# Performance work log

Hardware: AMD Instinct MI355X
Metric: run time of the kernel (lower is better)

Reference implementation:

```python
import jax, jax.numpy as jnp
from jax import lax
import numpy as np

N_TAGS = 16      # number of pos-tag experts
N_PRI = 4        # first N_PRI tags are privacy terms
UNK_ID = 0
VOCAB = 40000    # parser word vocabulary
M = 1024         # per-tag target vocab size
E = 100          # parser embedding dim
WED = 200        # word embedding dim (input encoder)
PED = 56         # pos embedding dim (input encoder)
H = 512          # ctx_fs (per-direction LSTM hidden)
TEMP = 1.0       # eval-mode gumbel temperature
ENT_PEN = 0.01


def _lstm(x, mask, Wx, Wh, b, reverse):
    # x: [B, L, D], mask: [B, L]; returns hidden states [B, L, H]
    B = x.shape[0]
    Hd = Wh.shape[0]
    gates_x = jnp.einsum('bld,dg->blg', x, Wx) + b  # precompute input part of gates

    def step(carry, inp):
        h, c = carry
        gx, m = inp  # gx: [B, 4H], m: [B, 1]
        gates = gx + h @ Wh
        i, f, g, o = jnp.split(gates, 4, axis=-1)
        i = jax.nn.sigmoid(i)
        f = jax.nn.sigmoid(f)
        g = jnp.tanh(g)
        o = jax.nn.sigmoid(o)
        c_new = f * c + i * g
        h_new = o * jnp.tanh(c_new)
        # masked update (padded steps keep previous state)
        h_new = h_new * m + h * (1.0 - m)
        c_new = c_new * m + c * (1.0 - m)
        return (h_new, c_new), h_new

    seq = (jnp.swapaxes(gates_x, 0, 1), jnp.swapaxes(mask, 0, 1)[..., None])
    init = (jnp.zeros((B, Hd), x.dtype), jnp.zeros((B, Hd), x.dtype))
    _, hs = lax.scan(step, init, seq, reverse=reverse)
    return jnp.swapaxes(hs, 0, 1)


def setup_inputs():
    key = jax.random.key(0)
    ks = jax.random.split(key, 16)
    B, L = 32, 256
    D = WED + PED  # 256
    inp = {}
    inp['inp_word'] = jax.random.randint(ks[0], (B, L), 0, VOCAB, dtype=jnp.int32)
    inp['inp_pos'] = jax.random.randint(ks[1], (B, L), 0, N_TAGS, dtype=jnp.int32)
    inp['inp_mask'] = jnp.ones((B, L), jnp.float32)
    inp['gumbel_u'] = jax.random.uniform(ks[2], (B * L, M), jnp.float32)
    inp['word_emb'] = jax.random.normal(ks[3], (VOCAB, WED), jnp.float32) * 0.1
    inp['pos_emb'] = jax.random.normal(ks[4], (N_TAGS, PED), jnp.float32) * 0.1
    inp['Wx_f'] = jax.random.normal(ks[5], (D, 4 * H), jnp.float32) * 0.05
    inp['Wh_f'] = jax.random.normal(ks[6], (H, 4 * H), jnp.float32) * 0.05
    inp['b_f'] = jnp.zeros((4 * H,), jnp.float32)
    inp['Wx_b'] = jax.random.normal(ks[7], (D, 4 * H), jnp.float32) * 0.05
    inp['Wh_b'] = jax.random.normal(ks[8], (H, 4 * H), jnp.float32) * 0.05
    inp['b_b'] = jnp.zeros((4 * H,), jnp.float32)
    inp['dec_W'] = jax.random.normal(ks[9], (N_TAGS, 2 * H, M), jnp.float32) * 0.03
    inp['dec_b'] = jnp.zeros((N_TAGS, M), jnp.float32)
    inp['words_tbl'] = jax.random.randint(ks[10], (N_TAGS, M), 0, VOCAB, dtype=jnp.int32)
    inp['psr_weight'] = jax.random.normal(ks[11], (VOCAB, E), jnp.float32) * 0.1
    return inp


def reference(inp_word, inp_pos, inp_mask, gumbel_u, word_emb, pos_emb,
              Wx_f, Wh_f, b_f, Wx_b, Wh_b, b_b, dec_W, dec_b, words_tbl, psr_weight):
    B, L = inp_word.shape
    # input encoder: word + pos embedding concat
    x = jnp.concatenate([word_emb[inp_word], pos_emb[inp_pos]], axis=-1)
    # bidirectional masked LSTM context
    hf = _lstm(x, inp_mask, Wx_f, Wh_f, b_f, reverse=False)
    hb = _lstm(x, inp_mask, Wx_b, Wh_b, b_b, reverse=True)
    ctx = jnp.concatenate([hf, hb], axis=-1).reshape(B * L, 2 * H)

    pos = inp_pos.reshape(-1)            # [T]
    wflat = inp_word.reshape(-1)         # [T]
    g = -jnp.log(-jnp.log(gumbel_u + 1e-10) + 1e-10)  # gumbel noise [T, M]

    obf_word = wflat
    obf_emb = psr_weight[wflat]          # [T, E]
    entropy = jnp.float32(0.0)
    for p in range(N_TAGS):  # loop over fixed small expert set
        m = pos == p                                    # routing mask [T]
        logp = jax.nn.log_softmax(ctx @ dec_W[p] + dec_b[p], axis=-1)  # [T, M]
        n = jnp.sum(m).astype(logp.dtype)
        ent_p = jnp.sum((-logp * jnp.exp(logp)) * m[:, None]) / jnp.maximum(n * M, 1.0)
        entropy = entropy + jnp.where(n > 0, ent_p, 0.0)
        spt = jax.nn.softmax((logp + g) / TEMP, axis=-1)  # gumbel-softmax sample
        widx = words_tbl[p][jnp.argmax(spt, axis=-1)]
        obf_word = jnp.where(m, widx, obf_word)
        emb = spt @ psr_weight[words_tbl[p]]              # [T, E]
        obf_emb = jnp.where(m[:, None], emb, obf_emb)

    obf_mask = pos < N_TAGS   # all tags are target tags
    pri_mask = pos < N_PRI
    avoid = (obf_word == wflat) & obf_mask
    obf_word = jnp.where(avoid, UNK_ID, obf_word)
    obf_emb = jnp.where(avoid[:, None], psr_weight[UNK_ID], obf_emb)
    ent_loss = -entropy * ENT_PEN
    return (obf_word.reshape(B, L), obf_emb.reshape(B, L, E),
            obf_mask.reshape(B, L), pri_mask.reshape(B, L), ent_loss)
```

## Files before the change

kernel.cpp:

```cpp
#include <hip/hip_runtime.h>
#include <math.h>
#include <cstdint>

#define BB 32
#define LL 256
#define TT 8192
#define DIN 256
#define WEDm 200
#define PEDm 56
#define HH 512
#define G4 2048
#define MM 1024
#define EE 100
#define NTAGS 16

__global__ void k_embed(const int* __restrict__ word, const int* __restrict__ posi,
                        const float* __restrict__ wemb, const float* __restrict__ pemb,
                        float* __restrict__ X) {
  int t = blockIdx.x;
  int c = threadIdx.x * 4;
  float4 v;
  if (c < WEDm) {
    int w = word[t];
    v = *(const float4*)(wemb + (size_t)w * WEDm + c);
  } else {
    int p = posi[t];
    v = *(const float4*)(pemb + (size_t)p * PEDm + (c - WEDm));
  }
  *(float4*)(X + (size_t)t * DIN + c) = v;
}

__global__ __launch_bounds__(256) void k_gemm_bias(const float* __restrict__ A,
    const float* __restrict__ W, const float* __restrict__ bias,
    float* __restrict__ C, int Mm, int Nn, int Kk) {
  __shared__ float As[16][68];
  __shared__ float Bs[16][64];
  int tid = threadIdx.x;
  int tx = tid & 15, ty = tid >> 4;
  int row0 = blockIdx.y * 64, col0 = blockIdx.x * 64;
  float acc[4][4] = {};
  for (int k0 = 0; k0 < Kk; k0 += 16) {
    int r = tid >> 2, c = (tid & 3) * 4;
    float4 av = *(const float4*)(A + (size_t)(row0 + r) * Kk + k0 + c);
    As[c + 0][r] = av.x; As[c + 1][r] = av.y; As[c + 2][r] = av.z; As[c + 3][r] = av.w;
    int r2 = tid >> 4, c2 = (tid & 15) * 4;
    float4 bv = *(const float4*)(W + (size_t)(k0 + r2) * Nn + col0 + c2);
    *(float4*)(&Bs[r2][c2]) = bv;
    __syncthreads();
#pragma unroll
    for (int kk = 0; kk < 16; ++kk) {
      float4 a4 = *(const float4*)(&As[kk][ty * 4]);
      float4 b4 = *(const float4*)(&Bs[kk][tx * 4]);
      float a[4] = {a4.x, a4.y, a4.z, a4.w};
      float b[4] = {b4.x, b4.y, b4.z, b4.w};
#pragma unroll
      for (int i = 0; i < 4; ++i)
#pragma unroll
        for (int j = 0; j < 4; ++j)
          acc[i][j] += a[i] * b[j];
    }
    __syncthreads();
  }
#pragma unroll
  for (int i = 0; i < 4; ++i) {
    int row = row0 + ty * 4 + i;
#pragma unroll
    for (int j = 0; j < 4; ++j) {
      int col = col0 + tx * 4 + j;
      C[(size_t)row * Nn + col] = acc[i][j] + bias[col];
    }
  }
}

template <int N>
__device__ __forceinline__ float ror_add(float x) {
  int xi = __float_as_int(x);
  int yi = __builtin_amdgcn_update_dpp(xi, xi, 0x100 + N, 0xF, 0xF, false);
  return x + __int_as_float(yi);
}

__device__ __forceinline__ float sigm(float x) { return 1.f / (1.f + __expf(-x)); }

__global__ __launch_bounds__(512, 1) void k_lstm6(
    const float* __restrict__ Whf, const float* __restrict__ Whb,
    const float* __restrict__ GXfp, const float* __restrict__ GXbp,
    const float* __restrict__ maskp, float* __restrict__ Hbuf,
    float* __restrict__ ctx, int* __restrict__ flags) {
  extern __shared__ float lds[];
  float* Wtmp = lds;
  float* Hs   = lds;
  float* part = lds + 8 * 516;
  const int tid = threadIdx.x;
  const int wg  = blockIdx.x;
  const int dir = wg & 1;
  const int bg  = (wg >> 1) & 3;
  const int ug  = wg >> 3;
  const int j0  = ug * 16;
  const int b0  = bg * 8;
  const float* Wh = dir ? Whb : Whf;
  const float* GX = dir ? GXbp : GXfp;

  const int ks = tid & 31;
  const int cq = tid >> 5;
  const int uu = tid & 15, bloc = tid >> 4;

  float4 wreg[4][4];
#pragma unroll
  for (int cc = 0; cc < 4; ++cc) {
    for (int i = tid; i < 16 * 512; i += 512) {
      int c = i >> 9, k = i & 511;
      Wtmp[c * 512 + k] = Wh[(size_t)k * G4 + cc * HH + j0 + c];
    }
    __syncthreads();
    if ((cq >> 2) == cc) {
      int cbase = (cq & 3) * 4;
#pragma unroll
      for (int ci = 0; ci < 4; ++ci)
#pragma unroll
        for (int j = 0; j < 4; ++j)
          wreg[ci][j] = *(const float4*)(Wtmp + (cbase + ci) * 512 + 4 * ks + 128 * j);
    }
    __syncthreads();
  }

  if (tid < 128) {
    __hip_atomic_store(&Hbuf[(size_t)(0 * 2 + dir) * 16384 + (b0 + bloc) * HH + j0 + uu],
                       0.f, __ATOMIC_RELAXED, __HIP_MEMORY_SCOPE_AGENT);
  }
  asm volatile("s_waitcnt vmcnt(0)" ::: "memory");
  __syncthreads();
  if (tid == 0)
    __hip_atomic_store(&flags[wg], 1, __ATOMIC_RELAXED, __HIP_MEMORY_SCOPE_AGENT);

  float cstate = 0.f;
  int par = 0;

  for (int s = 0; s < LL; ++s) {
    const int t = dir ? (LL - 1 - s) : s;

    float gx0 = 0.f, gx1 = 0.f, gx2 = 0.f, gx3 = 0.f, mval = 0.f;
    if (tid < 128) {
      const float* gp = GX + ((size_t)((b0 + bloc) * LL + t)) * G4 + j0 + uu;
      gx0 = gp[0]; gx1 = gp[512]; gx2 = gp[1024]; gx3 = gp[1536];
      mval = maskp[(b0 + bloc) * LL + t];
    }

    if (tid < 32) {
      int it = 0;
      while (__hip_atomic_load(&flags[(tid * 4 + bg) * 2 + dir], __ATOMIC_RELAXED,
                               __HIP_MEMORY_SCOPE_AGENT) < s + 1) {
        __builtin_amdgcn_s_sleep(1);
        if (++it > (1 << 20)) break;
      }
    }
    __syncthreads();
    __builtin_amdgcn_sched_barrier(0);

    {
      const unsigned long long* hb64 =
          (const unsigned long long*)(Hbuf + (size_t)(par * 2 + dir) * 16384 + b0 * HH);
      unsigned long long hv[4];
#pragma unroll
      for (int m = 0; m < 4; ++m)
        hv[m] = __hip_atomic_load(&hb64[tid + 512 * m], __ATOMIC_RELAXED,
                                  __HIP_MEMORY_SCOPE_AGENT);
#pragma unroll
      for (int m = 0; m < 4; ++m) {
        int f = 2 * (tid + 512 * m);
        int b = f >> 9, k = f & 511;
        *(float2*)(&Hs[b * 516 + k]) = *(float2*)(&hv[m]);
      }
    }
    __syncthreads();

    float acc[4][8];
#pragma unroll
    for (int ci = 0; ci < 4; ++ci)
#pragma unroll
      for (int bi = 0; bi < 8; ++bi) acc[ci][bi] = 0.f;
    {
      const float* hp = Hs + 4 * ks;
#pragma unroll
      for (int j = 0; j < 4; ++j) {
        const int ko = 128 * j;
        float4 h4[8];
#pragma unroll
        for (int bi = 0; bi < 8; ++bi) h4[bi] = *(const float4*)(hp + bi * 516 + ko);
#pragma unroll
        for (int ci = 0; ci < 4; ++ci) {
          float4 w = wreg[ci][j];
#pragma unroll
          for (int bi = 0; bi < 8; ++bi) {
            float4 h = h4[bi];
            acc[ci][bi] += w.x * h.x + w.y * h.y + w.z * h.z + w.w * h.w;
          }
        }
      }
    }
#pragma unroll
    for (int ci = 0; ci < 4; ++ci)
#pragma unroll
      for (int bi = 0; bi < 8; ++bi) {
        float v = acc[ci][bi];
        v = ror_add<1>(v); v = ror_add<2>(v); v = ror_add<4>(v); v = ror_add<8>(v);
        acc[ci][bi] = v;
      }
    if ((ks & 15) == 0) {
      const int ph = ks >> 4;
      float* dst = part + ph * 768 + (cq * 4) * 12;
#pragma unroll
      for (int ci = 0; ci < 4; ++ci) {
        *(float4*)(dst + ci * 12 + 0) = make_float4(acc[ci][0], acc[ci][1], acc[ci][2], acc[ci][3]);
        *(float4*)(dst + ci * 12 + 4) = make_float4(acc[ci][4], acc[ci][5], acc[ci][6], acc[ci][7]);
      }
    }
    __syncthreads();

    float hn = 0.f;
    if (tid < 128) {
      float pre[4];
#pragma unroll
      for (int q = 0; q < 4; ++q) {
        int lc = q * 16 + uu;
        pre[q] = part[lc * 12 + bloc] + part[768 + lc * 12 + bloc];
      }
      pre[0] += gx0; pre[1] += gx1; pre[2] += gx2; pre[3] += gx3;
      float gi = sigm(pre[0]);
      float gf = sigm(pre[1]);
      float gg = tanhf(pre[2]);
      float go = sigm(pre[3]);
      float cnew = gf * cstate + gi * gg;
      float hnew = go * tanhf(cnew);
      float hold = Hs[bloc * 516 + j0 + uu];
      hn = hnew * mval + hold * (1.f - mval);
      cstate = cnew * mval + cstate * (1.f - mval);
      __hip_atomic_store(&Hbuf[(size_t)((par ^ 1) * 2 + dir) * 16384 + (b0 + bloc) * HH + j0 + uu],
                         hn, __ATOMIC_RELAXED, __HIP_MEMORY_SCOPE_AGENT);
    }
    asm volatile("s_waitcnt vmcnt(0)" ::: "memory");
    __syncthreads();
    if (tid == 0)
      __hip_atomic_store(&flags[wg], s + 2, __ATOMIC_RELAXED, __HIP_MEMORY_SCOPE_AGENT);
    if (tid < 128)
      ctx[((size_t)((b0 + bloc) * LL + t)) * (2 * HH) + dir * HH + j0 + uu] = hn;
    par ^= 1;
  }
}

__global__ void k_init0(int* __restrict__ flags) { flags[threadIdx.x] = 0; }

__global__ void k_zero16(int* counts) { if (threadIdx.x < 16) counts[threadIdx.x] = 0; }

__global__ void k_count(const int* __restrict__ posi, int* __restrict__ counts) {
  int t = blockIdx.x * 256 + threadIdx.x;
  if (t < TT) atomicAdd(&counts[posi[t]], 1);
}

__global__ void k_prefix(const int* __restrict__ counts, int* __restrict__ offs) {
  if (threadIdx.x == 0) {
    int a = 0;
    for (int p = 0; p < NTAGS; ++p) { offs[p] = a; a += counts[p]; }
    offs[NTAGS] = a;
  }
}

__global__ __launch_bounds__(256) void k_compact(const int* __restrict__ posi,
    const int* __restrict__ offs, int* __restrict__ idxlist) {
  int p = blockIdx.x, tid = threadIdx.x;
  __shared__ int sc[256];
  __shared__ int sbase;
  if (tid == 0) sbase = offs[p];
  __syncthreads();
  for (int c0 = 0; c0 < TT; c0 += 256) {
    int t = c0 + tid;
    int f = (posi[t] == p) ? 1 : 0;
    int v = f;
    sc[tid] = v;
    __syncthreads();
    for (int o = 1; o < 256; o <<= 1) {
      int add = (tid >= o) ? sc[tid - o] : 0;
      __syncthreads();
      v += add;
      sc[tid] = v;
      __syncthreads();
    }
    int total = sc[255];
    int base = sbase;
    if (f) idxlist[base + v - 1] = t;
    __syncthreads();
    if (tid == 0) sbase = base + total;
    __syncthreads();
  }
}

__global__ void k_ptbl(const int* __restrict__ wtbl, const float* __restrict__ psrw,
                       float* __restrict__ Ptbl) {
  int i = blockIdx.x * 256 + threadIdx.x;
  int total = NTAGS * MM * EE;
  for (; i < total; i += gridDim.x * 256) {
    int p = i / (MM * EE);
    int rem = i - p * (MM * EE);
    int r = rem / EE;
    int e = rem - r * EE;
    Ptbl[i] = psrw[(size_t)wtbl[p * MM + r] * EE + e];
  }
}

__global__ __launch_bounds__(256) void k_decgemm(const float* __restrict__ ctxb,
    const float* __restrict__ decW, const float* __restrict__ decb,
    const int* __restrict__ counts, const int* __restrict__ offs,
    const int* __restrict__ idxlist, float* __restrict__ Z) {
  int p = blockIdx.z;
  int n = counts[p];
  int r0 = blockIdx.y * 64;
  if (r0 >= n) return;
  int col0 = blockIdx.x * 64;
  __shared__ float As[16][68];
  __shared__ float Bs[16][64];
  __shared__ int rows[64];
  int tid = threadIdx.x;
  if (tid < 64) {
    int r = r0 + tid;
    rows[tid] = idxlist[offs[p] + (r < n ? r : 0)];
  }
  __syncthreads();
  const float* W = decW + (size_t)p * MM * MM;
  float acc[4][4] = {};
  for (int k0 = 0; k0 < MM; k0 += 16) {
    int r = tid >> 2, c = (tid & 3) * 4;
    float4 av = *(const float4*)(ctxb + (size_t)rows[r] * MM + k0 + c);
    As[c + 0][r] = av.x; As[c + 1][r] = av.y; As[c + 2][r] = av.z; As[c + 3][r] = av.w;
    int r2 = tid >> 4, c2 = (tid & 15) * 4;
    float4 bv = *(const float4*)(W + (size_t)(k0 + r2) * MM + col0 + c2);
    *(float4*)(&Bs[r2][c2]) = bv;
    __syncthreads();
#pragma unroll
    for (int kk = 0; kk < 16; ++kk) {
      float4 a4 = *(const float4*)(&As[kk][(tid >> 4) * 4]);
      float4 b4 = *(const float4*)(&Bs[kk][(tid & 15) * 4]);
      float a[4] = {a4.x, a4.y, a4.z, a4.w};
      float b[4] = {b4.x, b4.y, b4.z, b4.w};
#pragma unroll
      for (int i = 0; i < 4; ++i)
#pragma unroll
        for (int j = 0; j < 4; ++j)
          acc[i][j] += a[i] * b[j];
    }
    __syncthreads();
  }
  int tx = tid & 15, ty = tid >> 4;
#pragma unroll
  for (int i = 0; i < 4; ++i) {
    int r = r0 + ty * 4 + i;
    if (r < n) {
      int tok = rows[ty * 4 + i];
#pragma unroll
      for (int j = 0; j < 4; ++j) {
        int col = col0 + tx * 4 + j;
        Z[(size_t)tok * MM + col] = acc[i][j] + decb[p * MM + col];
      }
    }
  }
}

__global__ __launch_bounds__(256) void k_softmax(
    const float* __restrict__ Z, const float* __restrict__ gum,
    const int* __restrict__ posi, const int* __restrict__ wflat,
    const int* __restrict__ wtbl, float* __restrict__ SPT,
    float* __restrict__ rowent, int* __restrict__ avoidb,
    float* __restrict__ out_word, float* __restrict__ out_mask,
    float* __restrict__ out_pri) {
  __shared__ float red[256];
  __shared__ float redv[256];
  __shared__ int redi[256];
  int t = blockIdx.x, tid = threadIdx.x;
  float z[4];
#pragma unroll
  for (int i = 0; i < 4; ++i) z[i] = Z[(size_t)t * MM + tid + 256 * i];
  float mx = fmaxf(fmaxf(z[0], z[1]), fmaxf(z[2], z[3]));
  red[tid] = mx; __syncthreads();
  for (int o = 128; o > 0; o >>= 1) { if (tid < o) red[tid] = fmaxf(red[tid], red[tid + o]); __syncthreads(); }
  mx = red[0]; __syncthreads();
  float se = 0.f;
#pragma unroll
  for (int i = 0; i < 4; ++i) se += expf(z[i] - mx);
  red[tid] = se; __syncthreads();
  for (int o = 128; o > 0; o >>= 1) { if (tid < o) red[tid] += red[tid + o]; __syncthreads(); }
  float lse = logf(red[0]); __syncthreads();
  float lp[4]; float ent = 0.f;
#pragma unroll
  for (int i = 0; i < 4; ++i) { lp[i] = z[i] - mx - lse; ent -= lp[i] * expf(lp[i]); }
  red[tid] = ent; __syncthreads();
  for (int o = 128; o > 0; o >>= 1) { if (tid < o) red[tid] += red[tid + o]; __syncthreads(); }
  float enttot = red[0]; __syncthreads();
  float y[4];
#pragma unroll
  for (int i = 0; i < 4; ++i) {
    float u = gum[(size_t)t * MM + tid + 256 * i];
    float g = -logf(-logf(u + 1e-10f) + 1e-10f);
    y[i] = lp[i] + g;
  }
  float bv = y[0]; int bi = tid;
#pragma unroll
  for (int i = 1; i < 4; ++i) { int j = tid + 256 * i; if (y[i] > bv) { bv = y[i]; bi = j; } }
  redv[tid] = bv; redi[tid] = bi; __syncthreads();
  for (int o = 128; o > 0; o >>= 1) {
    if (tid < o) {
      float v2 = redv[tid + o]; int i2 = redi[tid + o];
      if (v2 > redv[tid] || (v2 == redv[tid] && i2 < redi[tid])) { redv[tid] = v2; redi[tid] = i2; }
    }
    __syncthreads();
  }
  float ymax = redv[0]; int amax = redi[0]; __syncthreads();
  float e[4]; float s2 = 0.f;
#pragma unroll
  for (int i = 0; i < 4; ++i) { e[i] = expf(y[i] - ymax); s2 += e[i]; }
  red[tid] = s2; __syncthreads();
  for (int o = 128; o > 0; o >>= 1) { if (tid < o) red[tid] += red[tid + o]; __syncthreads(); }
  float inv = 1.f / red[0];
#pragma unroll
  for (int i = 0; i < 4; ++i) SPT[(size_t)t * MM + tid + 256 * i] = e[i] * inv;
  if (tid == 0) {
    int p = posi[t];
    int widx = wtbl[p * MM + amax];
    int wf = wflat[t];
    int avoid = (widx == wf) ? 1 : 0;
    avoidb[t] = avoid;
    out_word[t] = (float)(avoid ? 0 : widx);
    out_mask[t] = 1.0f;
    out_pri[t] = (p < 4) ? 1.0f : 0.0f;
    rowent[t] = enttot;
  }
}

__global__ __launch_bounds__(256) void k_embgemm(const float* __restrict__ SPT,
    const float* __restrict__ Ptbl, const float* __restrict__ psrw,
    const int* __restrict__ counts, const int* __restrict__ offs,
    const int* __restrict__ idxlist, const int* __restrict__ avoidb,
    float* __restrict__ out_emb) {
  int p = blockIdx.y;
  int n = counts[p];
  int r0 = blockIdx.x * 64;
  if (r0 >= n) return;
  __shared__ float As[16][68];
  __shared__ float Bs[16][132];
  __shared__ int rows[64];
  int tid = threadIdx.x;
  if (tid < 64) rows[tid] = idxlist[offs[p] + ((r0 + tid) < n ? (r0 + tid) : 0)];
  __syncthreads();
  const float* P = Ptbl + (size_t)p * MM * EE;
  int tx = tid & 31, ty = tid >> 5;
  float acc[8][4] = {};
  for (int k0 = 0; k0 < MM; k0 += 16) {
    int r = tid >> 2, c = (tid & 3) * 4;
    float4 av = *(const float4*)(SPT + (size_t)rows[r] * MM + k0 + c);
    As[c + 0][r] = av.x; As[c + 1][r] = av.y; As[c + 2][r] = av.z; As[c + 3][r] = av.w;
    int r2 = tid >> 4;
    int c2 = (tid & 15) * 8;
    float4 b0 = make_float4(0.f, 0.f, 0.f, 0.f), b1 = make_float4(0.f, 0.f, 0.f, 0.f);
    if (c2 + 3 < EE) b0 = *(const float4*)(P + (size_t)(k0 + r2) * EE + c2);
    if (c2 + 7 < EE) b1 = *(const float4*)(P + (size_t)(k0 + r2) * EE + c2 + 4);
    *(float4*)(&Bs[r2][c2]) = b0;
    *(float4*)(&Bs[r2][c2 + 4]) = b1;
    __syncthreads();
#pragma unroll
    for (int kk = 0; kk < 16; ++kk) {
      float4 b4 = *(const float4*)(&Bs[kk][tx * 4]);
      float4 a0 = *(const float4*)(&As[kk][ty * 8]);
      float4 a1 = *(const float4*)(&As[kk][ty * 8 + 4]);
      float a[8] = {a0.x, a0.y, a0.z, a0.w, a1.x, a1.y, a1.z, a1.w};
#pragma unroll
      for (int ri = 0; ri < 8; ++ri) {
        acc[ri][0] += a[ri] * b4.x; acc[ri][1] += a[ri] * b4.y;
        acc[ri][2] += a[ri] * b4.z; acc[ri][3] += a[ri] * b4.w;
      }
    }
    __syncthreads();
  }
#pragma unroll
  for (int ri = 0; ri < 8; ++ri) {
    int r = ty * 8 + ri;
    if (r0 + r < n) {
      int tok = rows[r];
      int av = avoidb[tok];
#pragma unroll
      for (int j = 0; j < 4; ++j) {
        int col = tx * 4 + j;
        if (col < EE) {
          float v = av ? psrw[col] : acc[ri][j];
          out_emb[(size_t)tok * EE + col] = v;
        }
      }
    }
  }
}

__global__ __launch_bounds__(256) void k_final(const float* __restrict__ rowent,
    const int* __restrict__ posi, const int* __restrict__ counts,
    float* __restrict__ out_loss) {
  __shared__ float red[256];
  int tid = threadIdx.x;
  float s = 0.f;
  for (int t = tid; t < TT; t += 256) {
    int p = posi[t];
    float denom = fmaxf((float)counts[p] * (float)MM, 1.0f);
    s += rowent[t] / denom;
  }
  red[tid] = s; __syncthreads();
  for (int o = 128; o > 0; o >>= 1) { if (tid < o) red[tid] += red[tid + o]; __syncthreads(); }
  if (tid == 0) out_loss[0] = -red[0] * 0.01f;
}

extern "C" void kernel_launch(void* const* d_in, const int* in_sizes, int n_in,
                              void* d_out, int out_size, void* d_ws, size_t ws_size,
                              hipStream_t stream) {
  const int*   inp_word = (const int*)d_in[0];
  const int*   inp_pos  = (const int*)d_in[1];
  const float* inp_mask = (const float*)d_in[2];
  const float* gum      = (const float*)d_in[3];
  const float* wemb     = (const float*)d_in[4];
  const float* pemb     = (const float*)d_in[5];
  const float* Wx_f     = (const float*)d_in[6];
  const float* Wh_f     = (const float*)d_in[7];
  const float* b_f      = (const float*)d_in[8];
  const float* Wx_b     = (const float*)d_in[9];
  const float* Wh_b     = (const float*)d_in[10];
  const float* b_b      = (const float*)d_in[11];
  const float* decW     = (const float*)d_in[12];
  const float* decb     = (const float*)d_in[13];
  const int*   wtbl     = (const int*)d_in[14];
  const float* psrw     = (const float*)d_in[15];

  float* out_word = (float*)d_out;
  float* out_emb  = out_word + TT;
  float* out_mask = out_emb + (size_t)TT * EE;
  float* out_pri  = out_mask + TT;
  float* out_loss = out_pri + TT;

  float* ws = (float*)d_ws;
  float* X      = ws;
  float* GXf    = X + (size_t)TT * DIN;
  float* GXb    = GXf + (size_t)TT * G4;
  float* ctxb   = GXb + (size_t)TT * G4;
  float* Hbuf   = ctxb + (size_t)TT * MM;
  float* rowent = Hbuf + 2 * 2 * BB * HH;
  int* avoidb   = (int*)(rowent + TT);
  int* counts   = avoidb + TT;
  int* offs     = counts + 16;
  int* idxlist  = offs + 32;
  int* flags    = idxlist + TT;
  float* Z    = GXf;
  float* SPT  = Z;
  float* Ptbl = GXb;

  k_embed<<<TT, 64, 0, stream>>>(inp_word, inp_pos, wemb, pemb, X);
  k_gemm_bias<<<dim3(G4 / 64, TT / 64), 256, 0, stream>>>(X, Wx_f, b_f, GXf, TT, G4, DIN);
  k_gemm_bias<<<dim3(G4 / 64, TT / 64), 256, 0, stream>>>(X, Wx_b, b_b, GXb, TT, G4, DIN);

  k_init0<<<1, 256, 0, stream>>>(flags);
  {
    const int ldsz = 32768;
    hipFuncSetAttribute((const void*)k_lstm6,
                        hipFuncAttributeMaxDynamicSharedMemorySize, ldsz);
    k_lstm6<<<256, 512, ldsz, stream>>>(Wh_f, Wh_b, GXf, GXb, inp_mask, Hbuf, ctxb, flags);
  }

  k_zero16<<<1, 64, 0, stream>>>(counts);
  k_count<<<TT / 256, 256, 0, stream>>>(inp_pos, counts);
  k_prefix<<<1, 64, 0, stream>>>(counts, offs);
  k_compact<<<NTAGS, 256, 0, stream>>>(inp_pos, offs, idxlist);
  k_ptbl<<<1024, 256, 0, stream>>>(wtbl, psrw, Ptbl);
  k_decgemm<<<dim3(MM / 64, TT / 64, NTAGS), 256, 0, stream>>>(ctxb, decW, decb, counts, offs, idxlist, Z);
  k_softmax<<<TT, 256, 0, stream>>>(Z, gum, inp_pos, inp_word, wtbl, SPT, rowent, avoidb,
                                    out_word, out_mask, out_pri);
  k_embgemm<<<dim3(TT / 64, NTAGS), 256, 0, stream>>>(SPT, Ptbl, psrw, counts, offs, idxlist,
                                                      avoidb, out_emb);
  k_final<<<1, 256, 0, stream>>>(rowent, inp_pos, counts, out_loss);
}
```

Baseline: 2.330 ms.

## Tag LSTM hidden state with step counters, merge input GEMMs, fuse softmax reductions

```diff
diff --git a/kernel.cpp b/kernel.cpp
--- a/kernel.cpp
+++ b/kernel.cpp
@@ -30,44 +30,57 @@
   *(float4*)(X + (size_t)t * DIN + c) = v;
 }
 
-__global__ __launch_bounds__(256) void k_gemm_bias(const float* __restrict__ A,
-    const float* __restrict__ W, const float* __restrict__ bias,
-    float* __restrict__ C, int Mm, int Nn, int Kk) {
-  __shared__ float As[16][68];
-  __shared__ float Bs[16][64];
-  int tid = threadIdx.x;
-  int tx = tid & 15, ty = tid >> 4;
-  int row0 = blockIdx.y * 64, col0 = blockIdx.x * 64;
-  float acc[4][4] = {};
-  for (int k0 = 0; k0 < Kk; k0 += 16) {
-    int r = tid >> 2, c = (tid & 3) * 4;
-    float4 av = *(const float4*)(A + (size_t)(row0 + r) * Kk + k0 + c);
-    As[c + 0][r] = av.x; As[c + 1][r] = av.y; As[c + 2][r] = av.z; As[c + 3][r] = av.w;
-    int r2 = tid >> 4, c2 = (tid & 15) * 4;
-    float4 bv = *(const float4*)(W + (size_t)(k0 + r2) * Nn + col0 + c2);
-    *(float4*)(&Bs[r2][c2]) = bv;
+__global__ __launch_bounds__(256) void k_gemm2(const float* __restrict__ X,
+    const float* __restrict__ Wf, const float* __restrict__ Wb,
+    const float* __restrict__ bf, const float* __restrict__ bb,
+    float* __restrict__ GXf, float* __restrict__ GXb) {
+  __shared__ float As[16][132];
+  __shared__ float Bs[16][132];
+  const int tid = threadIdx.x;
+  const int row0 = blockIdx.y * 128;
+  const int col0 = blockIdx.x * 128;
+  const int isB = (col0 >= G4) ? 1 : 0;
+  const float* W = isB ? Wb : Wf;
+  const float* bias = isB ? bb : bf;
+  const int wcol0 = col0 - (isB ? G4 : 0);
+  const int ar = tid >> 1, ac = (tid & 1) * 8;
+  const int br = tid >> 4, bc = (tid & 15) * 8;
+  const int ty = tid >> 4, tx = tid & 15;
+  float acc[8][8] = {};
+  for (int k0 = 0; k0 < DIN; k0 += 16) {
+    float4 a0 = *(const float4*)(X + (size_t)(row0 + ar) * DIN + k0 + ac);
+    float4 a1 = *(const float4*)(X + (size_t)(row0 + ar) * DIN + k0 + ac + 4);
+    float4 b0 = *(const float4*)(W + (size_t)(k0 + br) * G4 + wcol0 + bc);
+    float4 b1 = *(const float4*)(W + (size_t)(k0 + br) * G4 + wcol0 + bc + 4);
+    As[ac + 0][ar] = a0.x; As[ac + 1][ar] = a0.y; As[ac + 2][ar] = a0.z; As[ac + 3][ar] = a0.w;
+    As[ac + 4][ar] = a1.x; As[ac + 5][ar] = a1.y; As[ac + 6][ar] = a1.z; As[ac + 7][ar] = a1.w;
+    *(float4*)(&Bs[br][bc]) = b0;
+    *(float4*)(&Bs[br][bc + 4]) = b1;
     __syncthreads();
 #pragma unroll
     for (int kk = 0; kk < 16; ++kk) {
-      float4 a4 = *(const float4*)(&As[kk][ty * 4]);
-      float4 b4 = *(const float4*)(&Bs[kk][tx * 4]);
-      float a[4] = {a4.x, a4.y, a4.z, a4.w};
-      float b[4] = {b4.x, b4.y, b4.z, b4.w};
-#pragma unroll
-      for (int i = 0; i < 4; ++i)
-#pragma unroll
-        for (int j = 0; j < 4; ++j)
+      float4 aa0 = *(const float4*)(&As[kk][ty * 8]);
+      float4 aa1 = *(const float4*)(&As[kk][ty * 8 + 4]);
+      float4 bb0 = *(const float4*)(&Bs[kk][tx * 8]);
+      float4 bb1 = *(const float4*)(&Bs[kk][tx * 8 + 4]);
+      float a[8] = {aa0.x, aa0.y, aa0.z, aa0.w, aa1.x, aa1.y, aa1.z, aa1.w};
+      float b[8] = {bb0.x, bb0.y, bb0.z, bb0.w, bb1.x, bb1.y, bb1.z, bb1.w};
+#pragma unroll
+      for (int i = 0; i < 8; ++i)
+#pragma unroll
+        for (int j = 0; j < 8; ++j)
           acc[i][j] += a[i] * b[j];
     }
     __syncthreads();
   }
-#pragma unroll
-  for (int i = 0; i < 4; ++i) {
-    int row = row0 + ty * 4 + i;
-#pragma unroll
-    for (int j = 0; j < 4; ++j) {
-      int col = col0 + tx * 4 + j;
-      C[(size_t)row * Nn + col] = acc[i][j] + bias[col];
+  float* OUT = isB ? GXb : GXf;
+#pragma unroll
+  for (int i = 0; i < 8; ++i) {
+    int row = row0 + ty * 8 + i;
+#pragma unroll
+    for (int j = 0; j < 8; ++j) {
+      int col = wcol0 + tx * 8 + j;
+      OUT[(size_t)row * G4 + col] = acc[i][j] + bias[col];
     }
   }
 }
@@ -81,11 +94,16 @@
 
 __device__ __forceinline__ float sigm(float x) { return 1.f / (1.f + __expf(-x)); }
 
-__global__ __launch_bounds__(512, 1) void k_lstm6(
+__global__ void k_initH(unsigned long long* __restrict__ Hpair) {
+  int i = blockIdx.x * 256 + threadIdx.x;
+  Hpair[i] = (i < 32768) ? 0ull : 0xFFFFFFFF00000000ull;
+}
+
+__global__ __launch_bounds__(512, 1) void k_lstm7(
     const float* __restrict__ Whf, const float* __restrict__ Whb,
     const float* __restrict__ GXfp, const float* __restrict__ GXbp,
-    const float* __restrict__ maskp, float* __restrict__ Hbuf,
-    float* __restrict__ ctx, int* __restrict__ flags) {
+    const float* __restrict__ maskp, unsigned long long* __restrict__ Hpair,
+    float* __restrict__ ctx) {
   extern __shared__ float lds[];
   float* Wtmp = lds;
   float* Hs   = lds;
@@ -123,17 +141,7 @@
     __syncthreads();
   }
 
-  if (tid < 128) {
-    __hip_atomic_store(&Hbuf[(size_t)(0 * 2 + dir) * 16384 + (b0 + bloc) * HH + j0 + uu],
-                       0.f, __ATOMIC_RELAXED, __HIP_MEMORY_SCOPE_AGENT);
-  }
-  asm volatile("s_waitcnt vmcnt(0)" ::: "memory");
-  __syncthreads();
-  if (tid == 0)
-    __hip_atomic_store(&flags[wg], 1, __ATOMIC_RELAXED, __HIP_MEMORY_SCOPE_AGENT);
-
   float cstate = 0.f;
-  int par = 0;
 
   for (int s = 0; s < LL; ++s) {
     const int t = dir ? (LL - 1 - s) : s;
@@ -145,31 +153,34 @@
       mval = maskp[(b0 + bloc) * LL + t];
     }
 
-    if (tid < 32) {
-      int it = 0;
-      while (__hip_atomic_load(&flags[(tid * 4 + bg) * 2 + dir], __ATOMIC_RELAXED,
-                               __HIP_MEMORY_SCOPE_AGENT) < s + 1) {
-        __builtin_amdgcn_s_sleep(1);
-        if (++it > (1 << 20)) break;
-      }
-    }
-    __syncthreads();
-    __builtin_amdgcn_sched_barrier(0);
-
+    const unsigned long long* hb =
+        Hpair + ((size_t)((s & 1) * 2 + dir) * 32 + b0) * 512;
+    unsigned long long hv[8];
+#pragma unroll
+    for (int m = 0; m < 8; ++m)
+      hv[m] = __hip_atomic_load(&hb[tid + 512 * m], __ATOMIC_RELAXED,
+                                __HIP_MEMORY_SCOPE_AGENT);
     {
-      const unsigned long long* hb64 =
-          (const unsigned long long*)(Hbuf + (size_t)(par * 2 + dir) * 16384 + b0 * HH);
-      unsigned long long hv[4];
-#pragma unroll
-      for (int m = 0; m < 4; ++m)
-        hv[m] = __hip_atomic_load(&hb64[tid + 512 * m], __ATOMIC_RELAXED,
-                                  __HIP_MEMORY_SCOPE_AGENT);
-#pragma unroll
-      for (int m = 0; m < 4; ++m) {
-        int f = 2 * (tid + 512 * m);
-        int b = f >> 9, k = f & 511;
-        *(float2*)(&Hs[b * 516 + k]) = *(float2*)(&hv[m]);
-      }
+      const unsigned expect = (unsigned)s;
+      int guard = 0;
+      for (;;) {
+        unsigned stale = 0u;
+#pragma unroll
+        for (int m = 0; m < 8; ++m)
+          if ((unsigned)(hv[m] >> 32) != expect) stale |= (1u << m);
+        if (!stale) break;
+        if (++guard > (1 << 15)) break;
+#pragma unroll
+        for (int m = 0; m < 8; ++m)
+          if (stale & (1u << m))
+            hv[m] = __hip_atomic_load(&hb[tid + 512 * m], __ATOMIC_RELAXED,
+                                      __HIP_MEMORY_SCOPE_AGENT);
+      }
+    }
+#pragma unroll
+    for (int m = 0; m < 8; ++m) {
+      int f = tid + 512 * m;
+      Hs[(f >> 9) * 516 + (f & 511)] = __uint_as_float((unsigned)hv[m]);
     }
     __syncthreads();
 
@@ -216,7 +227,6 @@
     }
     __syncthreads();
 
-    float hn = 0.f;
     if (tid < 128) {
       float pre[4];
 #pragma unroll
@@ -232,22 +242,18 @@
       float cnew = gf * cstate + gi * gg;
       float hnew = go * tanhf(cnew);
       float hold = Hs[bloc * 516 + j0 + uu];
-      hn = hnew * mval + hold * (1.f - mval);
+      float hn = hnew * mval + hold * (1.f - mval);
       cstate = cnew * mval + cstate * (1.f - mval);
-      __hip_atomic_store(&Hbuf[(size_t)((par ^ 1) * 2 + dir) * 16384 + (b0 + bloc) * HH + j0 + uu],
-                         hn, __ATOMIC_RELAXED, __HIP_MEMORY_SCOPE_AGENT);
-    }
-    asm volatile("s_waitcnt vmcnt(0)" ::: "memory");
-    __syncthreads();
-    if (tid == 0)
-      __hip_atomic_store(&flags[wg], s + 2, __ATOMIC_RELAXED, __HIP_MEMORY_SCOPE_AGENT);
-    if (tid < 128)
+      unsigned long long pk = ((unsigned long long)(unsigned)(s + 1) << 32) |
+                              (unsigned long long)__float_as_uint(hn);
+      __hip_atomic_store(
+          &Hpair[((size_t)(((s + 1) & 1) * 2 + dir) * 32 + (b0 + bloc)) * 512 + j0 + uu],
+          pk, __ATOMIC_RELAXED, __HIP_MEMORY_SCOPE_AGENT);
       ctx[((size_t)((b0 + bloc) * LL + t)) * (2 * HH) + dir * HH + j0 + uu] = hn;
-    par ^= 1;
-  }
-}
-
-__global__ void k_init0(int* __restrict__ flags) { flags[threadIdx.x] = 0; }
+    }
+    __syncthreads();
+  }
+}
 
 __global__ void k_zero16(int* counts) { if (threadIdx.x < 16) counts[threadIdx.x] = 0; }
 
@@ -371,6 +377,7 @@
     float* __restrict__ out_word, float* __restrict__ out_mask,
     float* __restrict__ out_pri) {
   __shared__ float red[256];
+  __shared__ float red2[256];
   __shared__ float redv[256];
   __shared__ int redi[256];
   int t = blockIdx.x, tid = threadIdx.x;
@@ -381,24 +388,27 @@
   red[tid] = mx; __syncthreads();
   for (int o = 128; o > 0; o >>= 1) { if (tid < o) red[tid] = fmaxf(red[tid], red[tid + o]); __syncthreads(); }
   mx = red[0]; __syncthreads();
-  float se = 0.f;
-#pragma unroll
-  for (int i = 0; i < 4; ++i) se += expf(z[i] - mx);
-  red[tid] = se; __syncthreads();
-  for (int o = 128; o > 0; o >>= 1) { if (tid < o) red[tid] += red[tid + o]; __syncthreads(); }
-  float lse = logf(red[0]); __syncthreads();
-  float lp[4]; float ent = 0.f;
-#pragma unroll
-  for (int i = 0; i < 4; ++i) { lp[i] = z[i] - mx - lse; ent -= lp[i] * expf(lp[i]); }
-  red[tid] = ent; __syncthreads();
-  for (int o = 128; o > 0; o >>= 1) { if (tid < o) red[tid] += red[tid + o]; __syncthreads(); }
-  float enttot = red[0]; __syncthreads();
+  float ev[4]; float se = 0.f, we = 0.f;
+#pragma unroll
+  for (int i = 0; i < 4; ++i) {
+    float d = z[i] - mx;
+    float e = expf(d);
+    ev[i] = e; se += e; we += d * e;
+  }
+  red[tid] = se; red2[tid] = we; __syncthreads();
+  for (int o = 128; o > 0; o >>= 1) {
+    if (tid < o) { red[tid] += red[tid + o]; red2[tid] += red2[tid + o]; }
+    __syncthreads();
+  }
+  float se_tot = red[0], we_tot = red2[0]; __syncthreads();
+  float lse = logf(se_tot);
+  float ent = lse - we_tot / se_tot;
   float y[4];
 #pragma unroll
   for (int i = 0; i < 4; ++i) {
     float u = gum[(size_t)t * MM + tid + 256 * i];
     float g = -logf(-logf(u + 1e-10f) + 1e-10f);
-    y[i] = lp[i] + g;
+    y[i] = (z[i] - mx) + g;
   }
   float bv = y[0]; int bi = tid;
 #pragma unroll
@@ -412,14 +422,14 @@
     __syncthreads();
   }
   float ymax = redv[0]; int amax = redi[0]; __syncthreads();
-  float e[4]; float s2 = 0.f;
-#pragma unroll
-  for (int i = 0; i < 4; ++i) { e[i] = expf(y[i] - ymax); s2 += e[i]; }
+  float e2[4]; float s2 = 0.f;
+#pragma unroll
+  for (int i = 0; i < 4; ++i) { e2[i] = expf(y[i] - ymax); s2 += e2[i]; }
   red[tid] = s2; __syncthreads();
   for (int o = 128; o > 0; o >>= 1) { if (tid < o) red[tid] += red[tid + o]; __syncthreads(); }
   float inv = 1.f / red[0];
 #pragma unroll
-  for (int i = 0; i < 4; ++i) SPT[(size_t)t * MM + tid + 256 * i] = e[i] * inv;
+  for (int i = 0; i < 4; ++i) SPT[(size_t)t * MM + tid + 256 * i] = e2[i] * inv;
   if (tid == 0) {
     int p = posi[t];
     int widx = wtbl[p * MM + amax];
@@ -429,7 +439,7 @@
     out_word[t] = (float)(avoid ? 0 : widx);
     out_mask[t] = 1.0f;
     out_pri[t] = (p < 4) ? 1.0f : 0.0f;
-    rowent[t] = enttot;
+    rowent[t] = ent;
   }
 }
 
@@ -542,27 +552,25 @@
   float* GXf    = X + (size_t)TT * DIN;
   float* GXb    = GXf + (size_t)TT * G4;
   float* ctxb   = GXb + (size_t)TT * G4;
-  float* Hbuf   = ctxb + (size_t)TT * MM;
-  float* rowent = Hbuf + 2 * 2 * BB * HH;
+  unsigned long long* Hpair = (unsigned long long*)(ctxb + (size_t)TT * MM);
+  float* rowent = (float*)(Hpair + 65536);
   int* avoidb   = (int*)(rowent + TT);
   int* counts   = avoidb + TT;
   int* offs     = counts + 16;
   int* idxlist  = offs + 32;
-  int* flags    = idxlist + TT;
   float* Z    = GXf;
   float* SPT  = Z;
   float* Ptbl = GXb;
 
   k_embed<<<TT, 64, 0, stream>>>(inp_word, inp_pos, wemb, pemb, X);
-  k_gemm_bias<<<dim3(G4 / 64, TT / 64), 256, 0, stream>>>(X, Wx_f, b_f, GXf, TT, G4, DIN);
-  k_gemm_bias<<<dim3(G4 / 64, TT / 64), 256, 0, stream>>>(X, Wx_b, b_b, GXb, TT, G4, DIN);
-
-  k_init0<<<1, 256, 0, stream>>>(flags);
+  k_gemm2<<<dim3(2 * G4 / 128, TT / 128), 256, 0, stream>>>(X, Wx_f, Wx_b, b_f, b_b, GXf, GXb);
+
+  k_initH<<<256, 256, 0, stream>>>(Hpair);
   {
     const int ldsz = 32768;
-    hipFuncSetAttribute((const void*)k_lstm6,
+    hipFuncSetAttribute((const void*)k_lstm7,
                         hipFuncAttributeMaxDynamicSharedMemorySize, ldsz);
-    k_lstm6<<<256, 512, ldsz, stream>>>(Wh_f, Wh_b, GXf, GXb, inp_mask, Hbuf, ctxb, flags);
+    k_lstm7<<<256, 512, ldsz, stream>>>(Wh_f, Wh_b, GXf, GXb, inp_mask, Hpair, ctxb);
   }
 
   k_zero16<<<1, 64, 0, stream>>>(counts);
```

Result: faster. 2.123 ms (-8.9%).
